# Optimization experiments

Hardware: AMD Instinct MI355X
Metric: run time of the kernel (lower is better)

## Reference

```python
import jax, jax.numpy as jnp
import numpy as np

B, S, D = 2, 2048, 2048
HQ, HK, HD = 16, 8, 128          # query heads, kv heads, head_dim
EPS = 1e-6
ROPE_THETA = 10000.0
SCALE = HD ** -0.5


def setup_inputs() -> dict:
    key = jax.random.key(0)
    ks = jax.random.split(key, 6)
    s = lambda fan_in: 1.0 / np.sqrt(fan_in)
    return {
        "hidden_states": jax.random.normal(ks[0], (B, S, D), jnp.float32),
        "positions": jnp.arange(S, dtype=jnp.int32),
        "Wq": jax.random.normal(ks[1], (D, HQ * HD), jnp.float32) * s(D),
        "Wk": jax.random.normal(ks[2], (D, HK * HD), jnp.float32) * s(D),
        "Wv": jax.random.normal(ks[3], (D, HK * HD), jnp.float32) * s(D),
        "Wo": jax.random.normal(ks[4], (HQ * HD, D), jnp.float32) * s(HQ * HD),
        "q_norm_w": jnp.ones((HD,), jnp.float32),
        "k_norm_w": jnp.ones((HD,), jnp.float32),
    }


def _rmsnorm(x, w):
    # RMSNorm over last (head_dim) axis, as in q_norm/k_norm
    var = jnp.mean(jnp.square(x), axis=-1, keepdims=True)
    return x * jax.lax.rsqrt(var + EPS) * w


def _rope(x, positions):
    # x: [B, S, H, HD]; rotate_half-style RoPE (Qwen3 convention)
    half = HD // 2
    inv_freq = 1.0 / (ROPE_THETA ** (jnp.arange(0, half, dtype=jnp.float32) / half))
    angles = positions.astype(jnp.float32)[:, None] * inv_freq[None, :]  # [S, half]
    cos = jnp.cos(angles)[None, :, None, :]  # [1, S, 1, half]
    sin = jnp.sin(angles)[None, :, None, :]
    x1, x2 = x[..., :half], x[..., half:]
    return jnp.concatenate([x1 * cos - x2 * sin, x2 * cos + x1 * sin], axis=-1)


def reference(hidden_states, positions, Wq, Wk, Wv, Wo, q_norm_w, k_norm_w):
    b, s, _ = hidden_states.shape
    q = (hidden_states @ Wq).reshape(b, s, HQ, HD)
    k = (hidden_states @ Wk).reshape(b, s, HK, HD)
    v = (hidden_states @ Wv).reshape(b, s, HK, HD)

    q = _rmsnorm(q, q_norm_w)
    k = _rmsnorm(k, k_norm_w)

    q = _rope(q, positions)
    k = _rope(k, positions)

    # GQA: repeat KV heads to match query heads
    groups = HQ // HK
    k = jnp.repeat(k, groups, axis=2)  # [B, S, HQ, HD]
    v = jnp.repeat(v, groups, axis=2)

    scores = jnp.einsum("bqhd,bkhd->bhqk", q, k) * SCALE  # [B, HQ, S, S]
    causal = jnp.tril(jnp.ones((s, s), dtype=bool))
    scores = jnp.where(causal[None, None], scores, jnp.float32(-jnp.inf))
    attn = jax.nn.softmax(scores, axis=-1)

    out = jnp.einsum("bhqk,bkhd->bqhd", attn, v).reshape(b, s, HQ * HD)
    return out @ Wo
```

## Files before the change

### kernel.cpp

```cpp
#include <hip/hip_runtime.h>
#include <cstdint>
#include <cstddef>

typedef _Float16 half8 __attribute__((ext_vector_type(8)));
typedef _Float16 half4 __attribute__((ext_vector_type(4)));
typedef float f32x4 __attribute__((ext_vector_type(4)));

#define DI __device__ __forceinline__

DI void gld_lds16(void* sp, const void* gp) {
  __builtin_amdgcn_global_load_lds(
      (const __attribute__((address_space(1))) void*)gp,
      (__attribute__((address_space(3))) void*)sp, 16, 0, 0);
}

__global__ __launch_bounds__(256) void prep(const float* __restrict__ hs,
                                            const float* __restrict__ Wq,
                                            const float* __restrict__ Wk,
                                            const float* __restrict__ Wv,
                                            const float* __restrict__ Wo,
                                            _Float16* __restrict__ Xh,
                                            _Float16* __restrict__ Wqkvt,
                                            _Float16* __restrict__ Wot) {
  const int bid = blockIdx.x;
  if (bid >= 12288) {
    const int i = (bid - 12288) * 256 + threadIdx.x;
    const float4* p = (const float4*)hs + (size_t)i * 2;
    const float4 a = p[0], b = p[1];
    half8 h;
    h[0] = (_Float16)a.x; h[1] = (_Float16)a.y; h[2] = (_Float16)a.z; h[3] = (_Float16)a.w;
    h[4] = (_Float16)b.x; h[5] = (_Float16)b.y; h[6] = (_Float16)b.z; h[7] = (_Float16)b.w;
    *(half8*)(Xh + (size_t)i * 8) = h;
    return;
  }
  const float* in;
  _Float16* outp;
  int C, t;
  if (bid < 4096)      { in = Wq; outp = Wqkvt;                        C = 2048; t = bid; }
  else if (bid < 6144) { in = Wk; outp = Wqkvt + (size_t)2048 * 2048;  C = 1024; t = bid - 4096; }
  else if (bid < 8192) { in = Wv; outp = Wqkvt + (size_t)3072 * 2048;  C = 1024; t = bid - 6144; }
  else                 { in = Wo; outp = Wot;                          C = 2048; t = bid - 8192; }
  __shared__ float tl[32][33];
  const int tx = threadIdx.x & 31, ty = threadIdx.x >> 5;
  const int ctiles = C >> 5;
  const int tc = t % ctiles, tr = t / ctiles;
  const int r0 = tr * 32, c0 = tc * 32;
#pragma unroll
  for (int i = 0; i < 4; i++)
    tl[ty + 8 * i][tx] = in[(size_t)(r0 + ty + 8 * i) * C + c0 + tx];
  __syncthreads();
#pragma unroll
  for (int i = 0; i < 4; i++) {
    const int rr = ty + 8 * i;
    outp[(size_t)(c0 + rr) * 2048 + r0 + tx] = (_Float16)tl[tx][rr];
  }
}

__global__ __launch_bounds__(256) void gemm_bt(const _Float16* __restrict__ A,
                                               const _Float16* __restrict__ Bt,
                                               float* __restrict__ C,
                                               int M, int N, int K) {
  __shared__ _Float16 sA[2][128 * 32];
  __shared__ _Float16 sB[2][128 * 32];
  const int tid = threadIdx.x;
  const int w = tid >> 6, l = tid & 63, lo = l & 15, hi = l >> 4;
  const int gx = gridDim.x, nwg = gx * gridDim.y;
  int bid = blockIdx.y * gx + blockIdx.x;
  bid = (bid & 7) * (nwg >> 3) + (bid >> 3);
  const int bn0 = (bid % gx) * 128, bm0 = (bid / gx) * 128;
  const int wm = w >> 1, wn = w & 1;
  const int srow = l >> 2;
  const int csel = ((l & 3) ^ ((l >> 3) & 3)) * 8;
  const int kswz = (hi ^ ((lo >> 1) & 3)) * 8;

  f32x4 acc[4][4];
#pragma unroll
  for (int mi = 0; mi < 4; mi++)
#pragma unroll
    for (int ni = 0; ni < 4; ni++)
#pragma unroll
      for (int r = 0; r < 4; r++) acc[mi][ni][r] = 0.0f;

  auto stage = [&](int bi, int kt) {
#pragma unroll
    for (int i = 0; i < 2; ++i) {
      const int j = 2 * w + i;
      gld_lds16(&sA[bi][j * 512],
                A + (size_t)(bm0 + j * 16 + srow) * K + (size_t)kt * 32 + csel);
      gld_lds16(&sB[bi][j * 512],
                Bt + (size_t)(bn0 + j * 16 + srow) * K + (size_t)kt * 32 + csel);
    }
  };

  stage(0, 0);
  __syncthreads();
  const int KT = K >> 5;
#pragma unroll 1
  for (int kt = 0; kt < KT; ++kt) {
    const int cur = kt & 1;
    if (kt + 1 < KT) stage(cur ^ 1, kt + 1);
    half8 a[4], b[4];
#pragma unroll
    for (int mi = 0; mi < 4; mi++)
      a[mi] = *(const half8*)&sA[cur][(wm * 64 + mi * 16 + lo) * 32 + kswz];
#pragma unroll
    for (int ni = 0; ni < 4; ni++)
      b[ni] = *(const half8*)&sB[cur][(wn * 64 + ni * 16 + lo) * 32 + kswz];
#pragma unroll
    for (int mi = 0; mi < 4; mi++)
#pragma unroll
      for (int ni = 0; ni < 4; ni++)
        acc[mi][ni] = __builtin_amdgcn_mfma_f32_16x16x32_f16(a[mi], b[ni], acc[mi][ni], 0, 0, 0);
    __syncthreads();
  }

#pragma unroll
  for (int mi = 0; mi < 4; mi++)
#pragma unroll
    for (int ni = 0; ni < 4; ni++)
#pragma unroll
      for (int r = 0; r < 4; r++)
        C[(size_t)(bm0 + wm * 64 + mi * 16 + hi * 4 + r) * N +
          (bn0 + wn * 64 + ni * 16 + lo)] = acc[mi][ni][r];
}

__global__ __launch_bounds__(256) void norm_rope(const float* __restrict__ QKV,
                                                 const int* __restrict__ pos,
                                                 const float* __restrict__ qw,
                                                 const float* __restrict__ kw,
                                                 _Float16* __restrict__ Qb,
                                                 _Float16* __restrict__ Kb) {
  const int w = threadIdx.x >> 6, l = threadIdx.x & 63;
  const int wv = blockIdx.x * 4 + w;
  const int t = wv / 24, hh = wv - t * 24;
  const int b = t >> 11, s = t & 2047;
  const bool isq = hh < 16;
  const int col = isq ? hh * 128 : 2048 + (hh - 16) * 128;
  const float* x = QKV + (size_t)t * 4096 + col;
  const float x1 = x[l], x2 = x[l + 64];
  float ss = x1 * x1 + x2 * x2;
  ss += __shfl_xor(ss, 32); ss += __shfl_xor(ss, 16); ss += __shfl_xor(ss, 8);
  ss += __shfl_xor(ss, 4);  ss += __shfl_xor(ss, 2);  ss += __shfl_xor(ss, 1);
  const float rn = rsqrtf(ss * 0.0078125f + 1e-6f);
  const float* wt = isq ? qw : kw;
  const float n1 = x1 * rn * wt[l], n2 = x2 * rn * wt[l + 64];
  const float ang = (float)pos[s] * exp2f((float)l * -0.2076205059304601f);
  float sa, ca;
  sincosf(ang, &sa, &ca);
  const float qs = isq ? 0.12751731f : 1.0f;
  const float o1 = (n1 * ca - n2 * sa) * qs;
  const float o2 = (n2 * ca + n1 * sa) * qs;
  _Float16* dst = isq ? Qb + (((size_t)b * 16 + hh) * 2048 + s) * 128
                      : Kb + (((size_t)b * 8 + (hh - 16)) * 2048 + s) * 128;
  dst[l] = (_Float16)o1;
  dst[l + 64] = (_Float16)o2;
}

__global__ __launch_bounds__(256) void v_trans(const float* __restrict__ QKV,
                                               _Float16* __restrict__ Vt) {
  __shared__ float t[32][33];
  const int tx = threadIdx.x & 31, ty = threadIdx.x >> 5;
  const int dt = blockIdx.x & 3;
  const int st = (blockIdx.x >> 2) & 63;
  const int bh = blockIdx.x >> 8;
  const float* src = QKV + (size_t)((bh >> 3) * 2048 + st * 32) * 4096 +
                     3072 + (bh & 7) * 128 + dt * 32;
#pragma unroll
  for (int i = 0; i < 4; i++)
    t[ty + 8 * i][tx] = src[(size_t)(ty + 8 * i) * 4096 + tx];
  __syncthreads();
  _Float16* dst = Vt + ((size_t)bh * 128 + dt * 32) * 2048 + st * 32;
#pragma unroll
  for (int i = 0; i < 4; i++) {
    const int rr = ty + 8 * i;
    dst[(size_t)rr * 2048 + tx] = (_Float16)t[tx][rr];
  }
}

__global__ __launch_bounds__(256) void attn_fwd(const _Float16* __restrict__ Q,
                                                const _Float16* __restrict__ K,
                                                const _Float16* __restrict__ Vt,
                                                _Float16* __restrict__ AO) {
  __shared__ _Float16 sK[2][64 * 128];
  __shared__ _Float16 sV[2][128 * 64];
  __shared__ _Float16 P[4][16 * 80];
  const int tid = threadIdx.x, w = tid >> 6, l = tid & 63, lo = l & 15, hi = l >> 4;
  const int qt = 31 - (blockIdx.x >> 5);
  const int hq = blockIdx.x & 15;
  const int b = (blockIdx.x >> 4) & 1;
  const int hk = hq >> 1, q0 = qt * 64;
  const _Float16* Qh = Q + ((size_t)(b * 16 + hq) * 2048) * 128;
  const _Float16* Kh = K + ((size_t)(b * 8 + hk) * 2048) * 128;
  const _Float16* Vh = Vt + ((size_t)(b * 8 + hk) * 128) * 2048;
  const int qw0 = q0 + w * 16;

  auto stageK = [&](int bi, int kv0) {
#pragma unroll
    for (int i = 0; i < 4; ++i) {
      const int inst = w * 4 + i;
      const int r = inst * 4 + (l >> 4);
      const int cb = ((l & 15) * 16) ^ ((r & 7) << 4);
      gld_lds16(&sK[bi][inst * 512],
                (const char*)Kh + (size_t)(kv0 + r) * 256 + cb);
    }
  };
  auto stageV = [&](int bi, int kv0) {
#pragma unroll
    for (int i = 0; i < 4; ++i) {
      const int inst = w * 4 + i;
      const int r = inst * 8 + (l >> 3);
      const int cb = ((l & 7) * 16) ^ ((r & 7) << 4);
      gld_lds16(&sV[bi][inst * 512],
                (const char*)Vh + (size_t)r * 4096 + (size_t)kv0 * 2 + cb);
    }
  };

  half8 aq[4];
#pragma unroll
  for (int kc = 0; kc < 4; kc++)
    aq[kc] = *(const half8*)(Qh + (size_t)(qw0 + lo) * 128 + kc * 32 + hi * 8);

  f32x4 o[8];
#pragma unroll
  for (int dn = 0; dn < 8; dn++)
#pragma unroll
    for (int r = 0; r < 4; r++) o[dn][r] = 0.0f;
  float mrow = -1e30f, lrow = 0.0f;

  const int nt = qt + 1;
  stageK(0, 0);
  stageV(0, 0);
  __syncthreads();
#pragma unroll 1
  for (int kt = 0; kt < nt; ++kt) {
    const int kv0 = kt * 64;
    const int cur = kt & 1;
    if (kt + 1 < nt) {
      stageK(cur ^ 1, kv0 + 64);
      stageV(cur ^ 1, kv0 + 64);
    }
    const char* kb = (const char*)sK[cur];
    const char* vb = (const char*)sV[cur];
    f32x4 s[4];
#pragma unroll
    for (int ns = 0; ns < 4; ns++) {
#pragma unroll
      for (int r = 0; r < 4; r++) s[ns][r] = 0.0f;
      const int krow = ns * 16 + lo;
#pragma unroll
      for (int kc = 0; kc < 4; kc++) {
        half8 bk = *(const half8*)(kb + krow * 256 +
                                   ((kc * 64 + hi * 16) ^ ((krow & 7) << 4)));
        s[ns] = __builtin_amdgcn_mfma_f32_16x16x32_f16(bk, aq[kc], s[ns], 0, 0, 0);
      }
    }
    if (kt == nt - 1) {
#pragma unroll
      for (int ns = 0; ns < 4; ns++) {
        const int kv = kv0 + ns * 16 + hi * 4;
#pragma unroll
        for (int r = 0; r < 4; r++)
          if (kv + r > qw0 + lo) s[ns][r] = -1e30f;
      }
    }
    float tmax = s[0][0];
#pragma unroll
    for (int ns = 0; ns < 4; ns++)
#pragma unroll
      for (int r = 0; r < 4; r++) tmax = fmaxf(tmax, s[ns][r]);
    tmax = fmaxf(tmax, __shfl_xor(tmax, 16));
    tmax = fmaxf(tmax, __shfl_xor(tmax, 32));
    if (!__all(tmax <= mrow + 8.0f)) {
      const float mn = fmaxf(mrow, tmax);
      const float corr = exp2f(mrow - mn);
      mrow = mn;
      lrow *= corr;
      float c4[4];
#pragma unroll
      for (int r = 0; r < 4; r++) c4[r] = __shfl(corr, hi * 4 + r, 16);
#pragma unroll
      for (int dn = 0; dn < 8; dn++)
#pragma unroll
        for (int r = 0; r < 4; r++) o[dn][r] *= c4[r];
    }
    float psum = 0.0f;
#pragma unroll
    for (int ns = 0; ns < 4; ns++) {
      half4 pk;
#pragma unroll
      for (int r = 0; r < 4; r++) {
        const float p = exp2f(s[ns][r] - mrow);
        psum += p;
        pk[r] = (_Float16)p;
      }
      *(half4*)&P[w][lo * 80 + ns * 16 + hi * 4] = pk;
    }
    psum += __shfl_xor(psum, 16);
    psum += __shfl_xor(psum, 32);
    lrow += psum;
    asm volatile("s_waitcnt lgkmcnt(0)" ::: "memory");
    half8 ap0 = *(const half8*)&P[w][lo * 80 + hi * 8];
    half8 ap1 = *(const half8*)&P[w][lo * 80 + 32 + hi * 8];
#pragma unroll
    for (int dn = 0; dn < 8; dn++) {
      const int vrow = dn * 16 + lo;
      half8 bv0 = *(const half8*)(vb + vrow * 128 + ((hi * 16) ^ ((vrow & 7) << 4)));
      half8 bv1 = *(const half8*)(vb + vrow * 128 + ((64 + hi * 16) ^ ((vrow & 7) << 4)));
      o[dn] = __builtin_amdgcn_mfma_f32_16x16x32_f16(ap0, bv0, o[dn], 0, 0, 0);
      o[dn] = __builtin_amdgcn_mfma_f32_16x16x32_f16(ap1, bv1, o[dn], 0, 0, 0);
    }
    __syncthreads();
  }

  const float inv = 1.0f / lrow;
  float i4[4];
#pragma unroll
  for (int r = 0; r < 4; r++) i4[r] = __shfl(inv, hi * 4 + r, 16);
  const size_t tok = (size_t)b * 2048 + qw0;
#pragma unroll
  for (int dn = 0; dn < 8; dn++)
#pragma unroll
    for (int r = 0; r < 4; r++)
      AO[(tok + hi * 4 + r) * 2048 + hq * 128 + dn * 16 + lo] = (_Float16)(o[dn][r] * i4[r]);
}

extern "C" void kernel_launch(void* const* d_in, const int* in_sizes, int n_in,
                              void* d_out, int out_size, void* d_ws, size_t ws_size,
                              hipStream_t stream) {
  (void)in_sizes; (void)n_in; (void)out_size; (void)ws_size;
  const float* hs  = (const float*)d_in[0];
  const int*   pos = (const int*)d_in[1];
  const float* Wq  = (const float*)d_in[2];
  const float* Wk  = (const float*)d_in[3];
  const float* Wv  = (const float*)d_in[4];
  const float* Wo  = (const float*)d_in[5];
  const float* qnw = (const float*)d_in[6];
  const float* knw = (const float*)d_in[7];
  float* out = (float*)d_out;

  char* ws = (char*)d_ws;
  size_t off = 0;
  auto take = [&](size_t bytes) -> void* {
    void* p = ws + off;
    off += (bytes + 255) & ~(size_t)255;
    return p;
  };
  _Float16* Xh    = (_Float16*)take((size_t)4096 * 2048 * 2);
  _Float16* Wqkvt = (_Float16*)take((size_t)4096 * 2048 * 2);
  _Float16* Wot   = (_Float16*)take((size_t)2048 * 2048 * 2);
  float*    QKV   = (float*)take((size_t)4096 * 4096 * 4);
  _Float16* Qb    = (_Float16*)take((size_t)2 * 16 * 2048 * 128 * 2);
  _Float16* Kb    = (_Float16*)take((size_t)2 * 8 * 2048 * 128 * 2);
  _Float16* Vt    = (_Float16*)take((size_t)2 * 8 * 128 * 2048 * 2);
  _Float16* AO    = (_Float16*)take((size_t)4096 * 2048 * 2);

  prep<<<16384, 256, 0, stream>>>(hs, Wq, Wk, Wv, Wo, Xh, Wqkvt, Wot);
  gemm_bt<<<dim3(32, 32), 256, 0, stream>>>(Xh, Wqkvt, QKV, 4096, 4096, 2048);
  norm_rope<<<24576, 256, 0, stream>>>(QKV, pos, qnw, knw, Qb, Kb);
  v_trans<<<4096, 256, 0, stream>>>(QKV, Vt);
  attn_fwd<<<1024, 256, 0, stream>>>(Qb, Kb, Vt, AO);
  gemm_bt<<<dim3(16, 32), 256, 0, stream>>>(AO, Wot, out, 4096, 2048, 2048);
}
```

Before: 252.3 us.

## Triple-buffer GEMM loads, emit fp16 QKV, fuse norm/rope with V transpose

The GEMM moves from double to triple buffering in LDS. It uses explicit vmcnt waits and raw barriers so that two K-tiles of loads stay in flight while MFMA runs. The QKV projection now writes fp16 instead of fp32, which halves that intermediate's write and read traffic. The norm/rope and V-transpose kernels merge into one launch. The cost is more LDS per block, which may lower occupancy, and an extra fp16 rounding of the pre-norm projections, which could cost some accuracy.

```diff
diff --git a/kernel.cpp b/kernel.cpp
--- a/kernel.cpp
+++ b/kernel.cpp
@@ -13,6 +13,9 @@
       (const __attribute__((address_space(1))) void*)gp,
       (__attribute__((address_space(3))) void*)sp, 16, 0, 0);
 }
+
+template <int N>
+DI void vmwait() { asm volatile("s_waitcnt vmcnt(%0)" :: "n"(N) : "memory"); }
 
 __global__ __launch_bounds__(256) void prep(const float* __restrict__ hs,
                                             const float* __restrict__ Wq,
@@ -56,12 +59,13 @@
   }
 }
 
+template <bool F16OUT>
 __global__ __launch_bounds__(256) void gemm_bt(const _Float16* __restrict__ A,
                                                const _Float16* __restrict__ Bt,
-                                               float* __restrict__ C,
+                                               void* __restrict__ Cv,
                                                int M, int N, int K) {
-  __shared__ _Float16 sA[2][128 * 32];
-  __shared__ _Float16 sB[2][128 * 32];
+  __shared__ _Float16 sA[3][128 * 32];
+  __shared__ _Float16 sB[3][128 * 32];
   const int tid = threadIdx.x;
   const int w = tid >> 6, l = tid & 63, lo = l & 15, hi = l >> 4;
   const int gx = gridDim.x, nwg = gx * gridDim.y;
@@ -81,7 +85,7 @@
 #pragma unroll
       for (int r = 0; r < 4; r++) acc[mi][ni][r] = 0.0f;
 
-  auto stage = [&](int bi, int kt) {
+  auto stage = [&](int kt, int bi) {
 #pragma unroll
     for (int i = 0; i < 2; ++i) {
       const int j = 2 * w + i;
@@ -93,12 +97,15 @@
   };
 
   stage(0, 0);
-  __syncthreads();
+  stage(1, 1);
+  vmwait<4>();
+  __builtin_amdgcn_s_barrier();
   const int KT = K >> 5;
+  int cur = 0;
 #pragma unroll 1
   for (int kt = 0; kt < KT; ++kt) {
-    const int cur = kt & 1;
-    if (kt + 1 < KT) stage(cur ^ 1, kt + 1);
+    const int nxt = (cur == 0) ? 2 : cur - 1;
+    if (kt + 2 < KT) stage(kt + 2, nxt);
     half8 a[4], b[4];
 #pragma unroll
     for (int mi = 0; mi < 4; mi++)
@@ -111,33 +118,61 @@
 #pragma unroll
       for (int ni = 0; ni < 4; ni++)
         acc[mi][ni] = __builtin_amdgcn_mfma_f32_16x16x32_f16(a[mi], b[ni], acc[mi][ni], 0, 0, 0);
+    if (kt + 2 < KT) vmwait<4>();
+    else if (kt + 2 == KT) vmwait<0>();
+    __builtin_amdgcn_s_barrier();
+    cur = (cur == 2) ? 0 : cur + 1;
+  }
+
+#pragma unroll
+  for (int mi = 0; mi < 4; mi++)
+#pragma unroll
+    for (int ni = 0; ni < 4; ni++)
+#pragma unroll
+      for (int r = 0; r < 4; r++) {
+        const size_t idx = (size_t)(bm0 + wm * 64 + mi * 16 + hi * 4 + r) * N +
+                           (bn0 + wn * 64 + ni * 16 + lo);
+        if constexpr (F16OUT) ((_Float16*)Cv)[idx] = (_Float16)acc[mi][ni][r];
+        else                  ((float*)Cv)[idx] = acc[mi][ni][r];
+      }
+}
+
+__global__ __launch_bounds__(256) void post(const _Float16* __restrict__ QKV,
+                                            const int* __restrict__ pos,
+                                            const float* __restrict__ qw,
+                                            const float* __restrict__ kw,
+                                            _Float16* __restrict__ Qb,
+                                            _Float16* __restrict__ Kb,
+                                            _Float16* __restrict__ Vt) {
+  if (blockIdx.x >= 24576) {
+    __shared__ _Float16 tt[32][33];
+    const int g = blockIdx.x - 24576;
+    const int tx = threadIdx.x & 31, ty = threadIdx.x >> 5;
+    const int dt = g & 3;
+    const int st = (g >> 2) & 63;
+    const int bh = g >> 8;
+    const _Float16* src = QKV + (size_t)((bh >> 3) * 2048 + st * 32) * 4096 +
+                          3072 + (bh & 7) * 128 + dt * 32;
+#pragma unroll
+    for (int i = 0; i < 4; i++)
+      tt[ty + 8 * i][tx] = src[(size_t)(ty + 8 * i) * 4096 + tx];
     __syncthreads();
-  }
-
-#pragma unroll
-  for (int mi = 0; mi < 4; mi++)
-#pragma unroll
-    for (int ni = 0; ni < 4; ni++)
-#pragma unroll
-      for (int r = 0; r < 4; r++)
-        C[(size_t)(bm0 + wm * 64 + mi * 16 + hi * 4 + r) * N +
-          (bn0 + wn * 64 + ni * 16 + lo)] = acc[mi][ni][r];
-}
-
-__global__ __launch_bounds__(256) void norm_rope(const float* __restrict__ QKV,
-                                                 const int* __restrict__ pos,
-                                                 const float* __restrict__ qw,
-                                                 const float* __restrict__ kw,
-                                                 _Float16* __restrict__ Qb,
-                                                 _Float16* __restrict__ Kb) {
+    _Float16* dst = Vt + ((size_t)bh * 128 + dt * 32) * 2048 + st * 32;
+#pragma unroll
+    for (int i = 0; i < 4; i++) {
+      const int rr = ty + 8 * i;
+      dst[(size_t)rr * 2048 + tx] = tt[tx][rr];
+    }
+    return;
+  }
   const int w = threadIdx.x >> 6, l = threadIdx.x & 63;
   const int wv = blockIdx.x * 4 + w;
   const int t = wv / 24, hh = wv - t * 24;
   const int b = t >> 11, s = t & 2047;
   const bool isq = hh < 16;
   const int col = isq ? hh * 128 : 2048 + (hh - 16) * 128;
-  const float* x = QKV + (size_t)t * 4096 + col;
-  const float x1 = x[l], x2 = x[l + 64];
+  const _Float16* x = QKV + (size_t)t * 4096 + col;
+  const float x1 = (float)x[l], x2 = (float)x[l + 64];
   float ss = x1 * x1 + x2 * x2;
   ss += __shfl_xor(ss, 32); ss += __shfl_xor(ss, 16); ss += __shfl_xor(ss, 8);
   ss += __shfl_xor(ss, 4);  ss += __shfl_xor(ss, 2);  ss += __shfl_xor(ss, 1);
@@ -156,27 +191,6 @@
   dst[l + 64] = (_Float16)o2;
 }
 
-__global__ __launch_bounds__(256) void v_trans(const float* __restrict__ QKV,
-                                               _Float16* __restrict__ Vt) {
-  __shared__ float t[32][33];
-  const int tx = threadIdx.x & 31, ty = threadIdx.x >> 5;
-  const int dt = blockIdx.x & 3;
-  const int st = (blockIdx.x >> 2) & 63;
-  const int bh = blockIdx.x >> 8;
-  const float* src = QKV + (size_t)((bh >> 3) * 2048 + st * 32) * 4096 +
-                     3072 + (bh & 7) * 128 + dt * 32;
-#pragma unroll
-  for (int i = 0; i < 4; i++)
-    t[ty + 8 * i][tx] = src[(size_t)(ty + 8 * i) * 4096 + tx];
-  __syncthreads();
-  _Float16* dst = Vt + ((size_t)bh * 128 + dt * 32) * 2048 + st * 32;
-#pragma unroll
-  for (int i = 0; i < 4; i++) {
-    const int rr = ty + 8 * i;
-    dst[(size_t)rr * 2048 + tx] = (_Float16)t[tx][rr];
-  }
-}
-
 __global__ __launch_bounds__(256) void attn_fwd(const _Float16* __restrict__ Q,
                                                 const _Float16* __restrict__ K,
                                                 const _Float16* __restrict__ Vt,
@@ -348,16 +362,15 @@
   _Float16* Xh    = (_Float16*)take((size_t)4096 * 2048 * 2);
   _Float16* Wqkvt = (_Float16*)take((size_t)4096 * 2048 * 2);
   _Float16* Wot   = (_Float16*)take((size_t)2048 * 2048 * 2);
-  float*    QKV   = (float*)take((size_t)4096 * 4096 * 4);
+  _Float16* QKVh  = (_Float16*)take((size_t)4096 * 4096 * 2);
   _Float16* Qb    = (_Float16*)take((size_t)2 * 16 * 2048 * 128 * 2);
   _Float16* Kb    = (_Float16*)take((size_t)2 * 8 * 2048 * 128 * 2);
   _Float16* Vt    = (_Float16*)take((size_t)2 * 8 * 128 * 2048 * 2);
   _Float16* AO    = (_Float16*)take((size_t)4096 * 2048 * 2);
 
   prep<<<16384, 256, 0, stream>>>(hs, Wq, Wk, Wv, Wo, Xh, Wqkvt, Wot);
-  gemm_bt<<<dim3(32, 32), 256, 0, stream>>>(Xh, Wqkvt, QKV, 4096, 4096, 2048);
-  norm_rope<<<24576, 256, 0, stream>>>(QKV, pos, qnw, knw, Qb, Kb);
-  v_trans<<<4096, 256, 0, stream>>>(QKV, Vt);
+  gemm_bt<true><<<dim3(32, 32), 256, 0, stream>>>(Xh, Wqkvt, QKVh, 4096, 4096, 2048);
+  post<<<28672, 256, 0, stream>>>(QKVh, pos, qnw, knw, Qb, Kb, Vt);
   attn_fwd<<<1024, 256, 0, stream>>>(Qb, Kb, Vt, AO);
-  gemm_bt<<<dim3(16, 32), 256, 0, stream>>>(AO, Wot, out, 4096, 2048, 2048);
-}
+  gemm_bt<false><<<dim3(16, 32), 256, 0, stream>>>(AO, Wot, out, 4096, 2048, 2048);
+}
```

New measurement: 263.6 us. 1.04x slower.
